# Performance work log

Hardware: AMD Instinct MI355X
Metric: run time of the kernel (lower is better)

## Reference

```python
import jax, jax.numpy as jnp
import numpy as np

SEQ_LEN = 4096
EMBED_DIM = 2048
NUM_HEADS = 16
HEAD_DIM = EMBED_DIM // NUM_HEADS


def setup_inputs() -> dict:
    key = jax.random.key(0)
    k1, k2, k3 = jax.random.split(key, 3)
    x = jax.random.normal(k1, (SEQ_LEN, EMBED_DIM), dtype=jnp.float32)
    # Dense-layer params (lecun-normal-ish scaling for stability)
    W_qkv = jax.random.normal(k2, (EMBED_DIM, 3 * EMBED_DIM), dtype=jnp.float32) / np.sqrt(EMBED_DIM)
    b_qkv = jnp.zeros((3 * EMBED_DIM,), dtype=jnp.float32)
    W_out = jax.random.normal(k3, (EMBED_DIM, EMBED_DIM), dtype=jnp.float32) / np.sqrt(EMBED_DIM)
    b_out = jnp.zeros((EMBED_DIM,), dtype=jnp.float32)
    return {"x": x, "W_qkv": W_qkv, "b_qkv": b_qkv, "W_out": W_out, "b_out": b_out}


def reference(x, W_qkv, b_qkv, W_out, b_out):
    seq_len = x.shape[0]
    qkv = x @ W_qkv + b_qkv                       # (S, 3E)
    qkv = qkv.reshape(seq_len, 3, NUM_HEADS, HEAD_DIM)
    q, k, v = qkv[:, 0], qkv[:, 1], qkv[:, 2]     # each (S, H, D)
    scale = 1.0 / jnp.sqrt(jnp.float32(HEAD_DIM))
    # NOTE: faithful to source -- contracts over BOTH heads and head_dim,
    # producing a single (S, S) attention matrix shared across heads.
    attn = jnp.einsum('thd,shd->ts', q, k) * scale
    causal = jnp.triu(jnp.ones((seq_len, seq_len), dtype=bool), k=1)
    attn = jnp.where(causal, -jnp.inf, attn)
    attn = jax.nn.softmax(attn, axis=-1)
    out = jnp.einsum('ts,shd->thd', attn, v)      # (S, H, D)
    out = out.reshape(seq_len, EMBED_DIM)
    return out @ W_out + b_out
```

## Files before the change

kernel.cpp:

```cpp
#include <hip/hip_runtime.h>
#include <cstdint>
#include <cstddef>

#define SEQLEN 4096
#define EMBED  2048
#define NH     16
#define HD     128
#define N3     6144
#define SCALE  0.08838834764831845f
#define MBIAS  25.0f

typedef __attribute__((ext_vector_type(8))) short bf16x8;
typedef __attribute__((ext_vector_type(4))) float f32x4;
typedef unsigned short u16;

#define MFMA(a, b, c) __builtin_amdgcn_mfma_f32_16x16x32_bf16((a), (b), (c), 0, 0, 0)

__device__ inline u16 f2bf(float f) {
  uint32_t u = __float_as_uint(f);
  u += 0x7FFF + ((u >> 16) & 1);
  return (u16)(u >> 16);
}

__device__ inline float bf2f(u16 u) {
  return __uint_as_float(((uint32_t)u) << 16);
}

__device__ inline void gload_lds16(const u16* g, u16* l) {
  __builtin_amdgcn_global_load_lds((const __attribute__((address_space(1))) void*)g,
                                   (__attribute__((address_space(3))) void*)l, 16, 0, 0);
}

__global__ __launch_bounds__(256) void conv_f32_bf16(const float* __restrict__ in,
                                                     u16* __restrict__ out, int n) {
  int i = (blockIdx.x * 256 + threadIdx.x) * 4;
  if (i >= n) return;
  float4 v = *(const float4*)(in + i);
  ushort4 o;
  o.x = f2bf(v.x); o.y = f2bf(v.y); o.z = f2bf(v.z); o.w = f2bf(v.w);
  *(ushort4*)(out + i) = o;
}

__global__ __launch_bounds__(256) void transpose_conv(const float* __restrict__ in,
                                                      u16* __restrict__ out, int R, int C) {
  __shared__ float t[32][33];
  int c0 = blockIdx.x * 32, r0 = blockIdx.y * 32;
  int tx = threadIdx.x, ty = threadIdx.y;
  #pragma unroll
  for (int i = ty; i < 32; i += 8)
    t[i][tx] = in[(size_t)(r0 + i) * C + c0 + tx];
  __syncthreads();
  #pragma unroll
  for (int i = ty; i < 32; i += 8)
    out[(size_t)(c0 + i) * R + r0 + tx] = f2bf(t[tx][i]);
}

__global__ __launch_bounds__(256) void vtrans(const u16* __restrict__ qkv, u16* __restrict__ vT) {
  __shared__ u16 t[32][33];
  int c0 = blockIdx.x * 32, t0 = blockIdx.y * 32;
  int tx = threadIdx.x, ty = threadIdx.y;
  #pragma unroll
  for (int i = ty; i < 32; i += 8)
    t[i][tx] = qkv[(size_t)(t0 + i) * N3 + 2 * EMBED + c0 + tx];
  __syncthreads();
  #pragma unroll
  for (int i = ty; i < 32; i += 8)
    vT[(size_t)(c0 + i) * SEQLEN + t0 + tx] = t[tx][i];
}

__global__ __launch_bounds__(256) void gemm_bt(const u16* __restrict__ A, const u16* __restrict__ Bt,
                                               const float* __restrict__ bias,
                                               u16* __restrict__ Cb, float* __restrict__ Cf,
                                               int M, int N, int K, int out_f32) {
  __shared__ __align__(16) u16 sA[128 * 32];
  __shared__ __align__(16) u16 sB[128 * 32];
  int tid = threadIdx.x;
  int bn = blockIdx.x, bm = blockIdx.y;
  int w = tid >> 6, l = tid & 63;
  int wr = w >> 1, wc = w & 1;
  int g = l >> 4, lr = l & 15;
  f32x4 acc[4][4] = {};
  int srow = tid >> 2, scol = (tid & 3) * 8;
  const u16* gA = A + (size_t)(bm * 128 + srow) * K + scol;
  const u16* gB = Bt + (size_t)(bn * 128 + srow) * K + scol;
  u16* lA = sA + srow * 32 + scol;
  u16* lB = sB + srow * 32 + scol;
  for (int kt = 0; kt < K; kt += 32) {
    gload_lds16(gA, lA);
    gload_lds16(gA + (size_t)64 * K, lA + 64 * 32);
    gload_lds16(gB, lB);
    gload_lds16(gB + (size_t)64 * K, lB + 64 * 32);
    gA += 32; gB += 32;
    __syncthreads();
    bf16x8 af[4], bfr[4];
    #pragma unroll
    for (int m = 0; m < 4; m++)
      af[m] = *(const bf16x8*)(sA + (wr * 64 + m * 16 + lr) * 32 + g * 8);
    #pragma unroll
    for (int n = 0; n < 4; n++)
      bfr[n] = *(const bf16x8*)(sB + (wc * 64 + n * 16 + lr) * 32 + g * 8);
    #pragma unroll
    for (int m = 0; m < 4; m++)
      #pragma unroll
      for (int n = 0; n < 4; n++)
        acc[m][n] = MFMA(af[m], bfr[n], acc[m][n]);
    __syncthreads();
  }
  int r0 = bm * 128 + wr * 64, c0 = bn * 128 + wc * 64;
  #pragma unroll
  for (int m = 0; m < 4; m++)
    #pragma unroll
    for (int n = 0; n < 4; n++) {
      int c = c0 + n * 16 + lr;
      float bv = bias[c];
      #pragma unroll
      for (int j = 0; j < 4; j++) {
        int r = r0 + m * 16 + g * 4 + j;
        float v = acc[m][n][j] + bv;
        if (out_f32) Cf[(size_t)r * N + c] = v;
        else         Cb[(size_t)r * N + c] = f2bf(v);
      }
    }
}

__global__ __launch_bounds__(256) void sgemm_p(const u16* __restrict__ qkv,
                                               u16* __restrict__ P) {
  int idx = blockIdx.x;
  int by = (int)((sqrtf(8.f * idx + 1.f) - 1.f) * 0.5f);
  while ((by + 1) * (by + 2) / 2 <= idx) by++;
  while (by * (by + 1) / 2 > idx) by--;
  int cx = idx - by * (by + 1) / 2;
  int r0g = by * 128, c0g = cx * 128;
  __shared__ __align__(16) u16 sA[128 * 32];
  __shared__ __align__(16) u16 sB[128 * 32];
  int tid = threadIdx.x;
  int w = tid >> 6, l = tid & 63;
  int wr = w >> 1, wc = w & 1;
  int g = l >> 4, lr = l & 15;
  f32x4 acc[4][4] = {};
  int srow = tid >> 2, scol = (tid & 3) * 8;
  const u16* gA = qkv + (size_t)(r0g + srow) * N3 + scol;
  const u16* gB = qkv + (size_t)(c0g + srow) * N3 + EMBED + scol;
  u16* lA = sA + srow * 32 + scol;
  u16* lB = sB + srow * 32 + scol;
  for (int kt = 0; kt < EMBED; kt += 32) {
    gload_lds16(gA, lA);
    gload_lds16(gA + (size_t)64 * N3, lA + 64 * 32);
    gload_lds16(gB, lB);
    gload_lds16(gB + (size_t)64 * N3, lB + 64 * 32);
    gA += 32; gB += 32;
    __syncthreads();
    bf16x8 af[4], bfr[4];
    #pragma unroll
    for (int m = 0; m < 4; m++)
      af[m] = *(const bf16x8*)(sA + (wr * 64 + m * 16 + lr) * 32 + g * 8);
    #pragma unroll
    for (int n = 0; n < 4; n++)
      bfr[n] = *(const bf16x8*)(sB + (wc * 64 + n * 16 + lr) * 32 + g * 8);
    #pragma unroll
    for (int m = 0; m < 4; m++)
      #pragma unroll
      for (int n = 0; n < 4; n++)
        acc[m][n] = MFMA(af[m], bfr[n], acc[m][n]);
    __syncthreads();
  }
  int r0 = r0g + wr * 64, c0 = c0g + wc * 64;
  #pragma unroll
  for (int m = 0; m < 4; m++)
    #pragma unroll
    for (int n = 0; n < 4; n++) {
      int c = c0 + n * 16 + lr;
      #pragma unroll
      for (int j = 0; j < 4; j++) {
        int r = r0 + m * 16 + g * 4 + j;
        float p = (c <= r) ? __expf(fmaf(acc[m][n][j], SCALE, -MBIAS)) : 0.f;
        P[(size_t)r * SEQLEN + c] = f2bf(p);
      }
    }
}

__global__ __launch_bounds__(256) void psum(const u16* __restrict__ P, float* __restrict__ L) {
  int wave = threadIdx.x >> 6, lane = threadIdx.x & 63;
  int r = blockIdx.x * 4 + wave;
  int ctop = ((r >> 7) + 1) * 128;
  const u16* Prow = P + (size_t)r * SEQLEN;
  float s = 0.f;
  for (int c = lane * 8; c < ctop; c += 512) {
    bf16x8 v = *(const bf16x8*)(Prow + c);
    #pragma unroll
    for (int j = 0; j < 8; j++) s += bf2f((u16)v[j]);
  }
  s += __shfl_xor(s, 1);  s += __shfl_xor(s, 2);  s += __shfl_xor(s, 4);
  s += __shfl_xor(s, 8);  s += __shfl_xor(s, 16); s += __shfl_xor(s, 32);
  if (lane == 0) L[r] = s;
}

__global__ __launch_bounds__(256) void pv_gemm(const u16* __restrict__ P,
                                               const u16* __restrict__ vT,
                                               const float* __restrict__ L,
                                               u16* __restrict__ O) {
  int by = 31 - blockIdx.y;
  int bx = blockIdx.x;
  int r0g = by * 128, c0g = bx * 64;
  int kend = r0g + 128;
  __shared__ __align__(16) u16 sA[128 * 32];
  __shared__ __align__(16) u16 sBv[64 * 32];
  int tid = threadIdx.x;
  int w = tid >> 6, l = tid & 63;
  int wr = w >> 1, wc = w & 1;
  int g = l >> 4, lr = l & 15;
  f32x4 acc[4][2] = {};
  int srow = tid >> 2, scol = (tid & 3) * 8;
  const u16* gA = P + (size_t)(r0g + srow) * SEQLEN + scol;
  u16* lA = sA + srow * 32 + scol;
  const u16* gB = vT + (size_t)(c0g + srow) * SEQLEN + scol;
  u16* lB = sBv + srow * 32 + scol;
  bool doB = srow < 64;
  for (int kt = 0; kt < kend; kt += 32) {
    gload_lds16(gA, lA);
    gload_lds16(gA + (size_t)64 * SEQLEN, lA + 64 * 32);
    if (doB) gload_lds16(gB, lB);
    gA += 32; gB += 32;
    __syncthreads();
    bf16x8 af[4], bfr[2];
    #pragma unroll
    for (int m = 0; m < 4; m++)
      af[m] = *(const bf16x8*)(sA + (wr * 64 + m * 16 + lr) * 32 + g * 8);
    #pragma unroll
    for (int n = 0; n < 2; n++)
      bfr[n] = *(const bf16x8*)(sBv + (wc * 32 + n * 16 + lr) * 32 + g * 8);
    #pragma unroll
    for (int m = 0; m < 4; m++)
      #pragma unroll
      for (int n = 0; n < 2; n++)
        acc[m][n] = MFMA(af[m], bfr[n], acc[m][n]);
    __syncthreads();
  }
  int r0 = r0g + wr * 64, c0 = c0g + wc * 32;
  #pragma unroll
  for (int m = 0; m < 4; m++) {
    float invl[4];
    #pragma unroll
    for (int j = 0; j < 4; j++)
      invl[j] = 1.f / L[r0 + m * 16 + g * 4 + j];
    #pragma unroll
    for (int n = 0; n < 2; n++) {
      int c = c0 + n * 16 + lr;
      #pragma unroll
      for (int j = 0; j < 4; j++) {
        int r = r0 + m * 16 + g * 4 + j;
        O[(size_t)r * EMBED + c] = f2bf(acc[m][n][j] * invl[j]);
      }
    }
  }
}

extern "C" void kernel_launch(void* const* d_in, const int* in_sizes, int n_in,
                              void* d_out, int out_size, void* d_ws, size_t ws_size,
                              hipStream_t stream) {
  const float* x     = (const float*)d_in[0];
  const float* W_qkv = (const float*)d_in[1];
  const float* b_qkv = (const float*)d_in[2];
  const float* W_out = (const float*)d_in[3];
  const float* b_out = (const float*)d_in[4];
  float* out = (float*)d_out;

  u16* xb    = (u16*)d_ws;
  u16* qkvb  = xb + (size_t)SEQLEN * EMBED;
  u16* Pbuf  = qkvb + (size_t)SEQLEN * N3;
  u16* vT    = Pbuf + (size_t)SEQLEN * SEQLEN;
  float* Lbuf = (float*)(vT + (size_t)EMBED * SEQLEN);
  u16* attb  = xb;
  u16* WqkvT = Pbuf;
  u16* WoutT = Pbuf;

  conv_f32_bf16<<<SEQLEN * EMBED / 1024, 256, 0, stream>>>(x, xb, SEQLEN * EMBED);
  transpose_conv<<<dim3(N3 / 32, EMBED / 32), dim3(32, 8), 0, stream>>>(W_qkv, WqkvT, EMBED, N3);
  gemm_bt<<<dim3(N3 / 128, SEQLEN / 128), 256, 0, stream>>>(xb, WqkvT, b_qkv, qkvb, nullptr,
                                                            SEQLEN, N3, EMBED, 0);
  vtrans<<<dim3(EMBED / 32, SEQLEN / 32), dim3(32, 8), 0, stream>>>(qkvb, vT);
  sgemm_p<<<528, 256, 0, stream>>>(qkvb, Pbuf);
  psum<<<SEQLEN / 4, 256, 0, stream>>>(Pbuf, Lbuf);
  pv_gemm<<<dim3(EMBED / 64, SEQLEN / 128), 256, 0, stream>>>(Pbuf, vT, Lbuf, attb);
  transpose_conv<<<dim3(EMBED / 32, EMBED / 32), dim3(32, 8), 0, stream>>>(W_out, WoutT, EMBED, EMBED);
  gemm_bt<<<dim3(EMBED / 128, SEQLEN / 128), 256, 0, stream>>>(attb, WoutT, b_out, nullptr, out,
                                                               SEQLEN, EMBED, EMBED, 1);
}
```

Before: 380.0 us.

## Unify GEMMs into triple-buffered 256x128 tile core with swizzled LDS

Replaces the three separate 128x128 single-buffered GEMM kernels (QKV projection, causal QK^T score, PV) with a shared 256x128 tile routine using 512 threads, a three-stage LDS ring buffer, and explicit vmcnt waits so global-to-LDS loads overlap MFMA work. LDS columns are XOR-swizzled to reduce bank conflicts, and MFMA sections run at raised wave priority. The causal score kernel now launches a full 2D grid with early exit for upper-triangle tiles, and the row-sum kernel is widened to match the 256-row causal boundary. This raises per-block LDS use and register pressure, and causal-tile granularity becomes coarser, so more masked-zero work is done.

Result: faster. 334.8 us (-11.9%).

```diff
diff --git a/kernel.cpp b/kernel.cpp
--- a/kernel.cpp
+++ b/kernel.cpp
@@ -9,6 +9,7 @@
 #define N3     6144
 #define SCALE  0.08838834764831845f
 #define MBIAS  25.0f
+#define LB3    12288
 
 typedef __attribute__((ext_vector_type(8))) short bf16x8;
 typedef __attribute__((ext_vector_type(4))) float f32x4;
@@ -29,6 +30,58 @@
 __device__ inline void gload_lds16(const u16* g, u16* l) {
   __builtin_amdgcn_global_load_lds((const __attribute__((address_space(1))) void*)g,
                                    (__attribute__((address_space(3))) void*)l, 16, 0, 0);
+}
+
+__device__ __forceinline__ void stage3(const u16* a0, const u16* a1, const u16* b0,
+                                       u16* base, int w, int lane) {
+  gload_lds16(a0, base + w * 512 + lane * 8);
+  gload_lds16(a1, base + 4096 + w * 512 + lane * 8);
+  gload_lds16(b0, base + 8192 + w * 512 + lane * 8);
+}
+
+__device__ __forceinline__ void mm256x128(const u16* gA, size_t sA, const u16* gB, size_t sB,
+                                          int NT, u16* lds, f32x4 (&acc)[4][4]) {
+  int tid = threadIdx.x;
+  int w = tid >> 6, lane = tid & 63;
+  int g = lane >> 4, lr = lane & 15;
+  int wm = w >> 1, wn = w & 1;
+  int arow = (w << 4) + (lane >> 2);
+  int cb = (((lane & 3) ^ (arow & 3)) << 3);
+  const u16* a0 = gA + (size_t)arow * sA + cb;
+  const u16* a1 = gA + (size_t)(128 + arow) * sA + cb;
+  const u16* b0 = gB + (size_t)arow * sB + cb;
+  int gx = ((g ^ (lr & 3)) << 3);
+  int aoff = ((wm << 6) + lr) * 32 + gx;
+  int boff = 8192 + ((wn << 6) + lr) * 32 + gx;
+  stage3(a0, a1, b0, lds, w, lane);
+  stage3(a0 + 32, a1 + 32, b0 + 32, lds + LB3, w, lane);
+  asm volatile("s_waitcnt vmcnt(3)" ::: "memory");
+  __builtin_amdgcn_s_barrier();
+  for (int t = 0; t < NT; ++t) {
+    u16* base = lds + (t % 3) * LB3;
+    bf16x8 af[4], bfr[4];
+    #pragma unroll
+    for (int m = 0; m < 4; m++) af[m] = *(const bf16x8*)(base + aoff + m * 512);
+    #pragma unroll
+    for (int n = 0; n < 4; n++) bfr[n] = *(const bf16x8*)(base + boff + n * 512);
+    if (t + 2 < NT) {
+      int kt = (t + 2) << 5;
+      stage3(a0 + kt, a1 + kt, b0 + kt, lds + ((t + 2) % 3) * LB3, w, lane);
+    }
+    __builtin_amdgcn_s_setprio(1);
+    #pragma unroll
+    for (int m = 0; m < 4; m++)
+      #pragma unroll
+      for (int n = 0; n < 4; n++)
+        acc[m][n] = MFMA(af[m], bfr[n], acc[m][n]);
+    __builtin_amdgcn_s_setprio(0);
+    if (t + 1 < NT) {
+      if (t + 2 < NT) asm volatile("s_waitcnt vmcnt(3)" ::: "memory");
+      else            asm volatile("s_waitcnt vmcnt(0)" ::: "memory");
+      __builtin_amdgcn_s_barrier();
+    }
+  }
+  asm volatile("" ::: "memory");
 }
 
 __global__ __launch_bounds__(256) void conv_f32_bf16(const float* __restrict__ in,
@@ -68,51 +121,24 @@
     vT[(size_t)(c0 + i) * SEQLEN + t0 + tx] = t[tx][i];
 }
 
-__global__ __launch_bounds__(256) void gemm_bt(const u16* __restrict__ A, const u16* __restrict__ Bt,
-                                               const float* __restrict__ bias,
-                                               u16* __restrict__ Cb, float* __restrict__ Cf,
-                                               int M, int N, int K, int out_f32) {
-  __shared__ __align__(16) u16 sA[128 * 32];
-  __shared__ __align__(16) u16 sB[128 * 32];
-  int tid = threadIdx.x;
+__global__ __launch_bounds__(512, 4) void gemm_bt2(const u16* __restrict__ A, const u16* __restrict__ Bt,
+                                                   const float* __restrict__ bias,
+                                                   u16* __restrict__ Cb, float* __restrict__ Cf,
+                                                   int M, int N, int K, int out_f32) {
+  __shared__ __align__(16) u16 lds[3 * LB3];
   int bn = blockIdx.x, bm = blockIdx.y;
-  int w = tid >> 6, l = tid & 63;
-  int wr = w >> 1, wc = w & 1;
-  int g = l >> 4, lr = l & 15;
   f32x4 acc[4][4] = {};
-  int srow = tid >> 2, scol = (tid & 3) * 8;
-  const u16* gA = A + (size_t)(bm * 128 + srow) * K + scol;
-  const u16* gB = Bt + (size_t)(bn * 128 + srow) * K + scol;
-  u16* lA = sA + srow * 32 + scol;
-  u16* lB = sB + srow * 32 + scol;
-  for (int kt = 0; kt < K; kt += 32) {
-    gload_lds16(gA, lA);
-    gload_lds16(gA + (size_t)64 * K, lA + 64 * 32);
-    gload_lds16(gB, lB);
-    gload_lds16(gB + (size_t)64 * K, lB + 64 * 32);
-    gA += 32; gB += 32;
-    __syncthreads();
-    bf16x8 af[4], bfr[4];
+  mm256x128(A + (size_t)(bm * 256) * K, K, Bt + (size_t)(bn * 128) * K, K, K >> 5, lds, acc);
+  int tid = threadIdx.x;
+  int w = tid >> 6, lane = tid & 63, g = lane >> 4, lr = lane & 15;
+  int wm = w >> 1, wn = w & 1;
+  int r0 = bm * 256 + wm * 64, c0 = bn * 128 + wn * 64;
+  #pragma unroll
+  for (int n = 0; n < 4; n++) {
+    int c = c0 + n * 16 + lr;
+    float bv = bias[c];
     #pragma unroll
     for (int m = 0; m < 4; m++)
-      af[m] = *(const bf16x8*)(sA + (wr * 64 + m * 16 + lr) * 32 + g * 8);
-    #pragma unroll
-    for (int n = 0; n < 4; n++)
-      bfr[n] = *(const bf16x8*)(sB + (wc * 64 + n * 16 + lr) * 32 + g * 8);
-    #pragma unroll
-    for (int m = 0; m < 4; m++)
-      #pragma unroll
-      for (int n = 0; n < 4; n++)
-        acc[m][n] = MFMA(af[m], bfr[n], acc[m][n]);
-    __syncthreads();
-  }
-  int r0 = bm * 128 + wr * 64, c0 = bn * 128 + wc * 64;
-  #pragma unroll
-  for (int m = 0; m < 4; m++)
-    #pragma unroll
-    for (int n = 0; n < 4; n++) {
-      int c = c0 + n * 16 + lr;
-      float bv = bias[c];
       #pragma unroll
       for (int j = 0; j < 4; j++) {
         int r = r0 + m * 16 + g * 4 + j;
@@ -120,51 +146,21 @@
         if (out_f32) Cf[(size_t)r * N + c] = v;
         else         Cb[(size_t)r * N + c] = f2bf(v);
       }
-    }
-}
-
-__global__ __launch_bounds__(256) void sgemm_p(const u16* __restrict__ qkv,
-                                               u16* __restrict__ P) {
-  int idx = blockIdx.x;
-  int by = (int)((sqrtf(8.f * idx + 1.f) - 1.f) * 0.5f);
-  while ((by + 1) * (by + 2) / 2 <= idx) by++;
-  while (by * (by + 1) / 2 > idx) by--;
-  int cx = idx - by * (by + 1) / 2;
-  int r0g = by * 128, c0g = cx * 128;
-  __shared__ __align__(16) u16 sA[128 * 32];
-  __shared__ __align__(16) u16 sB[128 * 32];
-  int tid = threadIdx.x;
-  int w = tid >> 6, l = tid & 63;
-  int wr = w >> 1, wc = w & 1;
-  int g = l >> 4, lr = l & 15;
+  }
+}
+
+__global__ __launch_bounds__(512, 4) void sgemm_p2(const u16* __restrict__ qkv,
+                                                   u16* __restrict__ P) {
+  int bx = blockIdx.x, by = blockIdx.y;
+  int r0g = by * 256, c0g = bx * 128;
+  if (c0g > r0g + 255) return;
+  __shared__ __align__(16) u16 lds[3 * LB3];
   f32x4 acc[4][4] = {};
-  int srow = tid >> 2, scol = (tid & 3) * 8;
-  const u16* gA = qkv + (size_t)(r0g + srow) * N3 + scol;
-  const u16* gB = qkv + (size_t)(c0g + srow) * N3 + EMBED + scol;
-  u16* lA = sA + srow * 32 + scol;
-  u16* lB = sB + srow * 32 + scol;
-  for (int kt = 0; kt < EMBED; kt += 32) {
-    gload_lds16(gA, lA);
-    gload_lds16(gA + (size_t)64 * N3, lA + 64 * 32);
-    gload_lds16(gB, lB);
-    gload_lds16(gB + (size_t)64 * N3, lB + 64 * 32);
-    gA += 32; gB += 32;
-    __syncthreads();
-    bf16x8 af[4], bfr[4];
-    #pragma unroll
-    for (int m = 0; m < 4; m++)
-      af[m] = *(const bf16x8*)(sA + (wr * 64 + m * 16 + lr) * 32 + g * 8);
-    #pragma unroll
-    for (int n = 0; n < 4; n++)
-      bfr[n] = *(const bf16x8*)(sB + (wc * 64 + n * 16 + lr) * 32 + g * 8);
-    #pragma unroll
-    for (int m = 0; m < 4; m++)
-      #pragma unroll
-      for (int n = 0; n < 4; n++)
-        acc[m][n] = MFMA(af[m], bfr[n], acc[m][n]);
-    __syncthreads();
-  }
-  int r0 = r0g + wr * 64, c0 = c0g + wc * 64;
+  mm256x128(qkv + (size_t)r0g * N3, N3, qkv + (size_t)c0g * N3 + EMBED, N3, EMBED >> 5, lds, acc);
+  int tid = threadIdx.x;
+  int w = tid >> 6, lane = tid & 63, g = lane >> 4, lr = lane & 15;
+  int wm = w >> 1, wn = w & 1;
+  int r0 = r0g + wm * 64, c0 = c0g + wn * 64;
   #pragma unroll
   for (int m = 0; m < 4; m++)
     #pragma unroll
@@ -182,7 +178,7 @@
 __global__ __launch_bounds__(256) void psum(const u16* __restrict__ P, float* __restrict__ L) {
   int wave = threadIdx.x >> 6, lane = threadIdx.x & 63;
   int r = blockIdx.x * 4 + wave;
-  int ctop = ((r >> 7) + 1) * 128;
+  int ctop = ((r >> 8) + 1) * 256;
   const u16* Prow = P + (size_t)r * SEQLEN;
   float s = 0.f;
   for (int c = lane * 8; c < ctop; c += 512) {
@@ -195,48 +191,20 @@
   if (lane == 0) L[r] = s;
 }
 
-__global__ __launch_bounds__(256) void pv_gemm(const u16* __restrict__ P,
-                                               const u16* __restrict__ vT,
-                                               const float* __restrict__ L,
-                                               u16* __restrict__ O) {
-  int by = 31 - blockIdx.y;
-  int bx = blockIdx.x;
-  int r0g = by * 128, c0g = bx * 64;
-  int kend = r0g + 128;
-  __shared__ __align__(16) u16 sA[128 * 32];
-  __shared__ __align__(16) u16 sBv[64 * 32];
-  int tid = threadIdx.x;
-  int w = tid >> 6, l = tid & 63;
-  int wr = w >> 1, wc = w & 1;
-  int g = l >> 4, lr = l & 15;
-  f32x4 acc[4][2] = {};
-  int srow = tid >> 2, scol = (tid & 3) * 8;
-  const u16* gA = P + (size_t)(r0g + srow) * SEQLEN + scol;
-  u16* lA = sA + srow * 32 + scol;
-  const u16* gB = vT + (size_t)(c0g + srow) * SEQLEN + scol;
-  u16* lB = sBv + srow * 32 + scol;
-  bool doB = srow < 64;
-  for (int kt = 0; kt < kend; kt += 32) {
-    gload_lds16(gA, lA);
-    gload_lds16(gA + (size_t)64 * SEQLEN, lA + 64 * 32);
-    if (doB) gload_lds16(gB, lB);
-    gA += 32; gB += 32;
-    __syncthreads();
-    bf16x8 af[4], bfr[2];
-    #pragma unroll
-    for (int m = 0; m < 4; m++)
-      af[m] = *(const bf16x8*)(sA + (wr * 64 + m * 16 + lr) * 32 + g * 8);
-    #pragma unroll
-    for (int n = 0; n < 2; n++)
-      bfr[n] = *(const bf16x8*)(sBv + (wc * 32 + n * 16 + lr) * 32 + g * 8);
-    #pragma unroll
-    for (int m = 0; m < 4; m++)
-      #pragma unroll
-      for (int n = 0; n < 2; n++)
-        acc[m][n] = MFMA(af[m], bfr[n], acc[m][n]);
-    __syncthreads();
-  }
-  int r0 = r0g + wr * 64, c0 = c0g + wc * 32;
+__global__ __launch_bounds__(512, 4) void pv_gemm2(const u16* __restrict__ P,
+                                                   const u16* __restrict__ vT,
+                                                   const float* __restrict__ L,
+                                                   u16* __restrict__ O) {
+  int bx = blockIdx.x, by = blockIdx.y;
+  int r0g = by * 256, c0g = bx * 128;
+  int NT = (r0g + 256) >> 5;
+  __shared__ __align__(16) u16 lds[3 * LB3];
+  f32x4 acc[4][4] = {};
+  mm256x128(P + (size_t)r0g * SEQLEN, SEQLEN, vT + (size_t)c0g * SEQLEN, SEQLEN, NT, lds, acc);
+  int tid = threadIdx.x;
+  int w = tid >> 6, lane = tid & 63, g = lane >> 4, lr = lane & 15;
+  int wm = w >> 1, wn = w & 1;
+  int r0 = r0g + wm * 64, c0 = c0g + wn * 64;
   #pragma unroll
   for (int m = 0; m < 4; m++) {
     float invl[4];
@@ -244,7 +212,7 @@
     for (int j = 0; j < 4; j++)
       invl[j] = 1.f / L[r0 + m * 16 + g * 4 + j];
     #pragma unroll
-    for (int n = 0; n < 2; n++) {
+    for (int n = 0; n < 4; n++) {
       int c = c0 + n * 16 + lr;
       #pragma unroll
       for (int j = 0; j < 4; j++) {
@@ -276,13 +244,13 @@
 
   conv_f32_bf16<<<SEQLEN * EMBED / 1024, 256, 0, stream>>>(x, xb, SEQLEN * EMBED);
   transpose_conv<<<dim3(N3 / 32, EMBED / 32), dim3(32, 8), 0, stream>>>(W_qkv, WqkvT, EMBED, N3);
-  gemm_bt<<<dim3(N3 / 128, SEQLEN / 128), 256, 0, stream>>>(xb, WqkvT, b_qkv, qkvb, nullptr,
-                                                            SEQLEN, N3, EMBED, 0);
+  gemm_bt2<<<dim3(N3 / 128, SEQLEN / 256), 512, 0, stream>>>(xb, WqkvT, b_qkv, qkvb, nullptr,
+                                                             SEQLEN, N3, EMBED, 0);
   vtrans<<<dim3(EMBED / 32, SEQLEN / 32), dim3(32, 8), 0, stream>>>(qkvb, vT);
-  sgemm_p<<<528, 256, 0, stream>>>(qkvb, Pbuf);
+  sgemm_p2<<<dim3(SEQLEN / 128, SEQLEN / 256), 512, 0, stream>>>(qkvb, Pbuf);
   psum<<<SEQLEN / 4, 256, 0, stream>>>(Pbuf, Lbuf);
-  pv_gemm<<<dim3(EMBED / 64, SEQLEN / 128), 256, 0, stream>>>(Pbuf, vT, Lbuf, attb);
+  pv_gemm2<<<dim3(EMBED / 128, SEQLEN / 256), 512, 0, stream>>>(Pbuf, vT, Lbuf, attb);
   transpose_conv<<<dim3(EMBED / 32, EMBED / 32), dim3(32, 8), 0, stream>>>(W_out, WoutT, EMBED, EMBED);
-  gemm_bt<<<dim3(EMBED / 128, SEQLEN / 128), 256, 0, stream>>>(attb, WoutT, b_out, nullptr, out,
-                                                               SEQLEN, EMBED, EMBED, 1);
-}
+  gemm_bt2<<<dim3(EMBED / 128, SEQLEN / 256), 512, 0, stream>>>(attb, WoutT, b_out, nullptr, out,
+                                                                SEQLEN, EMBED, EMBED, 1);
+}
```
